# Kernel optimization log

Measured on AMD Instinct MI355X. Metric: run time of the kernel, lower is better.

## Reference

```python
import jax, jax.numpy as jnp
import numpy as np


def _init(key, shape, fan_in):
    return jax.random.normal(key, shape, jnp.float32) * (1.0 / np.sqrt(fan_in))


def setup_inputs() -> dict:
    key = jax.random.key(0)
    ks = jax.random.split(key, 12)
    b, n, vd, ad, sd, hd = 32, 2048, 512, 128, 128, 64
    return {
        'vfeat': jax.random.normal(ks[0], (b, n, vd), jnp.float32),
        'afeat': jax.random.normal(ks[1], (b, n, ad), jnp.float32),
        'vfc_w': _init(ks[2], (ad, vd), vd), 'vfc_b': jnp.zeros((ad,), jnp.float32),
        'afc_w': _init(ks[3], (ad, ad), ad), 'afc_b': jnp.zeros((ad,), jnp.float32),
        'am_v_w': _init(ks[4], (sd, sd), sd), 'am_v_b': jnp.zeros((sd,), jnp.float32),
        'am_a_w': _init(ks[5], (sd, sd), sd), 'am_a_b': jnp.zeros((sd,), jnp.float32),
        'am_o_w': _init(ks[6], (1, sd), sd), 'am_o_b': jnp.zeros((1,), jnp.float32),
        'V_w': _init(ks[7], (hd, sd), sd), 'V_b': jnp.zeros((hd,), jnp.float32),
        'W_w': _init(ks[8], (1, hd), hd), 'W_b': jnp.zeros((1,), jnp.float32),
        'cls_w': _init(ks[9], (2, sd), sd), 'cls_b': jnp.zeros((2,), jnp.float32),
    }


def reference(vfeat, afeat, vfc_w, vfc_b, afc_w, afc_b,
              am_v_w, am_v_b, am_a_w, am_a_b, am_o_w, am_o_b,
              V_w, V_b, W_w, W_b, cls_w, cls_b):
    relu = jax.nn.relu
    # vfc / afc projections (dropout is identity in eval mode)
    vo1 = relu(jnp.einsum('bnd,kd->bnk', vfeat, vfc_w) + vfc_b)  # (b,n,128)
    ax = relu(jnp.einsum('bnd,kd->bnk', afeat, afc_w) + afc_b)   # (b,n,128)
    # AM(128): additive gated cross-modal attention: out = sigmoid(Wo tanh(Wv v + Wa a)) * a
    h = jnp.tanh(jnp.einsum('bnk,jk->bnj', vo1, am_v_w) + am_v_b
                 + jnp.einsum('bnk,jk->bnj', ax, am_a_w) + am_a_b)
    att = jax.nn.sigmoid(jnp.einsum('bnj,oj->bno', h, am_o_w) + am_o_b)  # (b,n,1)
    ffeat = att * ax + vo1  # attfeat + vo1, (b,n,128)
    # NOTE: original uses self.V for BOTH f_v and f_u (source bug kept)
    f_v = relu(jnp.einsum('bnk,hk->bnh', ffeat, V_w) + V_b)  # (b,n,64)
    f_u = f_v
    # W is affine with no nonlinearity on (fv_i + fu_j), so
    # W(fv_i + fu_j) = w.fv_i + w.fu_j + b  -- exact rank-1 decomposition
    s_v = f_v @ W_w[0]  # (b,n)
    s_u = f_u @ W_w[0]  # (b,n)
    pair = s_v[:, :, None] + s_u[:, None, :] + W_b[0]  # (b,n_i,n_j)
    p = jax.nn.softmax(pair, axis=1)  # F.softmax(scores, 0) per bag: over i
    scores = p.mean(axis=2)  # mean over j -> (b,n)
    # eval mode: training-only softmax over dim 2 skipped
    zfeat = jnp.einsum('bn,bnk->bk', scores, ffeat)  # (b,128)
    logits = zfeat @ cls_w.T + cls_b  # (b,2)
    return scores, logits
```

## Files before the change

kernel.cpp:

```cpp
#include <hip/hip_runtime.h>
#include <cstddef>
#include <cstdint>


typedef __attribute__((ext_vector_type(8))) short short8;
typedef __attribute__((ext_vector_type(4))) float float4v;

#define MFMA16(a, b, c) __builtin_amdgcn_mfma_f32_16x16x32_bf16((a), (b), (c), 0, 0, 0)

__device__ __forceinline__ unsigned short f2bf(float f) {
    union { float f; unsigned u; } v; v.f = f;
    unsigned r = (v.u + 0x7fffu + ((v.u >> 16) & 1u)) >> 16;
    return (unsigned short)r;
}
__device__ __forceinline__ float bf2f(unsigned short h) {
    union { unsigned u; float f; } v; v.u = ((unsigned)h) << 16;
    return v.f;
}
__device__ __forceinline__ float bf2f_s(short h) { return bf2f((unsigned short)h); }

__device__ __forceinline__ void bfsplit(float x, short& h, short& l) {
    union { float f; unsigned u; } v; v.f = x;
    h = (short)(v.u >> 16);
    union { unsigned u; float f; } hv; hv.u = v.u & 0xffff0000u;
    union { float f; unsigned u; } lv; lv.f = x - hv.f;
    l = (short)(lv.u >> 16);
}

__device__ __forceinline__ float tanh_fast(float x) {
    float e = __builtin_exp2f(x * 2.885390081777927f);
    return 1.f - 2.f / (e + 1.f);
}
__device__ __forceinline__ float sigmoid_fast(float x) {
    return 1.f / (1.f + __builtin_exp2f(-x * 1.4426950408889634f));
}

__device__ __forceinline__ void gload_lds16(const void* g, void* l) {
#if __has_builtin(__builtin_amdgcn_global_load_lds)
    __builtin_amdgcn_global_load_lds(
        (const __attribute__((address_space(1))) unsigned int*)g,
        (__attribute__((address_space(3))) unsigned int*)l, 16, 0, 0);
#else
    *(uint4*)l = *(const uint4*)g;
#endif
}

__global__ __launch_bounds__(256)
void prep(const float* __restrict__ vfc_w, const float* __restrict__ afc_w,
          const float* __restrict__ am_v_w, const float* __restrict__ am_a_w,
          const float* __restrict__ V_w,
          unsigned short* __restrict__ W1h, unsigned short* __restrict__ W1l,
          unsigned short* __restrict__ W1bh, unsigned short* __restrict__ W1bl,
          unsigned short* __restrict__ W2v, unsigned short* __restrict__ W2a,
          unsigned short* __restrict__ W3)
{
    int t = blockIdx.x * 256 + threadIdx.x;
    if (t < 65536) {
        int j = t & 7, lane = (t >> 3) & 63, ks = (t >> 9) & 15, nf = (t >> 13) & 7;
        int n = (lane & 15) + 16 * nf, k = ks * 32 + (lane >> 4) * 8 + j;
        float x = vfc_w[n * 512 + k];
        unsigned short h = f2bf(x);
        W1h[t] = h; W1l[t] = f2bf(x - bf2f(h));
    } else if (t < 81920) {
        int u = t - 65536;
        int j = u & 7, lane = (u >> 3) & 63, ks = (u >> 9) & 3, nf = (u >> 11) & 7;
        int n = (lane & 15) + 16 * nf, k = ks * 32 + (lane >> 4) * 8 + j;
        float x = afc_w[n * 128 + k];
        unsigned short h = f2bf(x);
        W1bh[u] = h; W1bl[u] = f2bf(x - bf2f(h));
    } else if (t < 98304) {
        int u = t - 81920;
        int j = u & 7, lane = (u >> 3) & 63, ks = (u >> 9) & 3, nf = (u >> 11) & 7;
        int n = (lane & 15) + 16 * nf, k = ks * 32 + (lane >> 4) * 8 + j;
        W2v[u] = f2bf(am_v_w[n * 128 + k]);
    } else if (t < 114688) {
        int u = t - 98304;
        int j = u & 7, lane = (u >> 3) & 63, ks = (u >> 9) & 3, nf = (u >> 11) & 7;
        int n = (lane & 15) + 16 * nf, k = ks * 32 + (lane >> 4) * 8 + j;
        W2a[u] = f2bf(am_a_w[n * 128 + k]);
    } else if (t < 122880) {
        int u = t - 114688;
        int j = u & 7, lane = (u >> 3) & 63, ks = (u >> 9) & 3, nf = (u >> 11) & 3;
        int n = (lane & 15) + 16 * nf, k = ks * 32 + (lane >> 4) * 8 + j;
        W3[u] = f2bf(V_w[n * 128 + k]);
    }
}

__global__ __launch_bounds__(256, 4)
void milA1(const float* __restrict__ vfeat, const float* __restrict__ vfc_b,
           const unsigned short* __restrict__ W1h,
           const unsigned short* __restrict__ W1l,
           float* __restrict__ vo1f)
{
    __shared__ __align__(16) unsigned short Abuf[2][4096];

    const int tid = threadIdx.x;
    const int lane = tid & 63, wid = tid >> 6;
    const int lr = lane & 15, lg = lane >> 4;
    const int rowbase = blockIdx.x * 64;
    const int nf0 = wid * 2;

    const float* sap = vfeat + (size_t)(rowbase + wid * 16 + (lane >> 2)) * 512
                       + (lane & 3) * 8;
    const int dlane = (lane >> 2) + 16 * (lane & 3);
    unsigned short* dh = &Abuf[0][0] + (wid * 2 + 0) * 512 + dlane * 8;
    unsigned short* dl = dh + 512;

    auto stage_write = [&](const float4 x0, const float4 x1, int buf) {
        const float xs[8] = {x0.x, x0.y, x0.z, x0.w, x1.x, x1.y, x1.z, x1.w};
        short8 h8, l8;
#pragma unroll
        for (int j = 0; j < 8; ++j) {
            short h, l; bfsplit(xs[j], h, l);
            h8[j] = h; l8[j] = l;
        }
        *(short8*)(dh + buf * 4096) = h8;
        *(short8*)(dl + buf * 4096) = l8;
    };

    float4v acc[4][2];
#pragma unroll
    for (int rf = 0; rf < 4; ++rf)
#pragma unroll
        for (int c = 0; c < 2; ++c)
#pragma unroll
            for (int i = 0; i < 4; ++i) acc[rf][c][i] = 0.f;

    {
        float4 x0 = *(const float4*)(sap);
        float4 x1 = *(const float4*)(sap + 4);
        stage_write(x0, x1, 0);
    }
    __syncthreads();

    for (int ks = 0; ks < 16; ++ks) {
        const int cur = ks & 1;
        float4 nx0, nx1;
        if (ks < 15) {
            nx0 = *(const float4*)(sap + (ks + 1) * 32);
            nx1 = *(const float4*)(sap + (ks + 1) * 32 + 4);
        }
        const short8 b0h = *(const short8*)(W1h + ((size_t)((nf0 + 0) * 16 + ks) * 64 + lane) * 8);
        const short8 b0l = *(const short8*)(W1l + ((size_t)((nf0 + 0) * 16 + ks) * 64 + lane) * 8);
        const short8 b1h = *(const short8*)(W1h + ((size_t)((nf0 + 1) * 16 + ks) * 64 + lane) * 8);
        const short8 b1l = *(const short8*)(W1l + ((size_t)((nf0 + 1) * 16 + ks) * 64 + lane) * 8);

#pragma unroll
        for (int rf = 0; rf < 4; ++rf) {
            const short8 ah = *(const short8*)&Abuf[cur][(rf * 2 + 0) * 512 + lane * 8];
            const short8 al = *(const short8*)&Abuf[cur][(rf * 2 + 1) * 512 + lane * 8];
            acc[rf][0] = MFMA16(ah, b0h, acc[rf][0]);
            acc[rf][0] = MFMA16(ah, b0l, acc[rf][0]);
            acc[rf][0] = MFMA16(al, b0h, acc[rf][0]);
            acc[rf][1] = MFMA16(ah, b1h, acc[rf][1]);
            acc[rf][1] = MFMA16(ah, b1l, acc[rf][1]);
            acc[rf][1] = MFMA16(al, b1h, acc[rf][1]);
        }
        if (ks < 15) stage_write(nx0, nx1, cur ^ 1);
        __syncthreads();
    }

#pragma unroll
    for (int c = 0; c < 2; ++c) {
        const float bb = vfc_b[lr + 16 * (nf0 + c)];
#pragma unroll
        for (int rf = 0; rf < 4; ++rf)
#pragma unroll
            for (int r = 0; r < 4; ++r)
                vo1f[(size_t)(rowbase + rf * 16 + lg * 4 + r) * 128 + lr + 16 * (nf0 + c)] =
                    fmaxf(acc[rf][c][r] + bb, 0.f);
    }
}

__global__ __launch_bounds__(256, 3)
void milA2(const float* __restrict__ afeat,
           const float* __restrict__ afc_b,
           const float* __restrict__ am_v_b, const float* __restrict__ am_a_b,
           const float* __restrict__ am_o_w, const float* __restrict__ am_o_b,
           const float* __restrict__ V_b, const float* __restrict__ W_w,
           const unsigned short* __restrict__ W1bh, const unsigned short* __restrict__ W1bl,
           const unsigned short* __restrict__ W2v, const unsigned short* __restrict__ W2a,
           const unsigned short* __restrict__ W3,
           float* vof,
           float* __restrict__ s_out)
{
    __shared__ __align__(16) unsigned short vo1s[8192];
    __shared__ __align__(16) unsigned short axs[8192];
    __shared__ __align__(16) unsigned short bstage[8192];

    const int tid = threadIdx.x;
    const int lane = tid & 63, wid = tid >> 6;
    const int lr = lane & 15, lg = lane >> 4;
    const int row0 = blockIdx.x * 64 + wid * 16;

    float vo1r[8][4];
#pragma unroll
    for (int nf = 0; nf < 8; ++nf)
#pragma unroll
        for (int r = 0; r < 4; ++r) {
            const float v = vof[(size_t)(row0 + lg * 4 + r) * 128 + lr + 16 * nf];
            vo1r[nf][r] = v;
            const int row = lg * 4 + r;
            const int col = lr + 16 * nf;
            vo1s[wid * 2048 + row * 128 + (col ^ ((row & 7) << 3))] = f2bf(v);
        }

    float4v acc1b[8];
#pragma unroll
    for (int nf = 0; nf < 8; ++nf)
#pragma unroll
        for (int i = 0; i < 4; ++i) acc1b[nf][i] = 0.f;

    {
        const float* ap = afeat + (size_t)(row0 + lr) * 128 + lg * 8;
        float4 a0[2], a1[2], a2[2];
        a0[0] = *(const float4*)(ap);      a0[1] = *(const float4*)(ap + 4);
        a1[0] = *(const float4*)(ap + 32); a1[1] = *(const float4*)(ap + 36);

        for (int ks = 0; ks < 4; ++ks) {
            __syncthreads();
#pragma unroll
            for (int i = 0; i < 4; ++i) {
                const int f = wid * 4 + i;
                const int nf = f & 7;
                const unsigned short* src = ((f >> 3) ? W1bl : W1bh)
                    + (size_t)(nf * 4 + ks) * 512 + (size_t)lane * 8;
                gload_lds16(src, &bstage[f * 512 + lane * 8]);
            }
            __syncthreads();

            if (ks < 2) {
                a2[0] = *(const float4*)(ap + (ks + 2) * 32);
                a2[1] = *(const float4*)(ap + (ks + 2) * 32 + 4);
            }
            short8 ah, al;
            {
                const float xs[8] = {a0[0].x, a0[0].y, a0[0].z, a0[0].w,
                                     a0[1].x, a0[1].y, a0[1].z, a0[1].w};
#pragma unroll
                for (int j = 0; j < 8; ++j) {
                    short h, l; bfsplit(xs[j], h, l);
                    ah[j] = h; al[j] = l;
                }
            }
#pragma unroll
            for (int nf = 0; nf < 8; ++nf) {
                const short8 bh = *(const short8*)&bstage[nf * 512 + lane * 8];
                const short8 bl = *(const short8*)&bstage[(8 + nf) * 512 + lane * 8];
                acc1b[nf] = MFMA16(ah, bh, acc1b[nf]);
                acc1b[nf] = MFMA16(ah, bl, acc1b[nf]);
                acc1b[nf] = MFMA16(al, bh, acc1b[nf]);
            }
            a0[0] = a1[0]; a0[1] = a1[1];
            a1[0] = a2[0]; a1[1] = a2[1];
        }
    }
#pragma unroll
    for (int nf = 0; nf < 8; ++nf) {
        const float bb = afc_b[lr + 16 * nf];
#pragma unroll
        for (int r = 0; r < 4; ++r) {
            float v = fmaxf(acc1b[nf][r] + bb, 0.f);
            acc1b[nf][r] = v;
            const int row = lg * 4 + r;
            const int col = lr + 16 * nf;
            axs[wid * 2048 + row * 128 + (col ^ ((row & 7) << 3))] = f2bf(v);
        }
    }

    float4v acc2[8];
#pragma unroll
    for (int nf = 0; nf < 8; ++nf)
#pragma unroll
        for (int i = 0; i < 4; ++i) acc2[nf][i] = 0.f;

    for (int ks = 0; ks < 4; ++ks) {
        __syncthreads();
#pragma unroll
        for (int i = 0; i < 4; ++i) {
            const int f = wid * 4 + i;
            const int nf = f & 7;
            const unsigned short* src = ((f >> 3) ? W2a : W2v)
                + (size_t)(nf * 4 + ks) * 512 + (size_t)lane * 8;
            gload_lds16(src, &bstage[f * 512 + lane * 8]);
        }
        __syncthreads();
        const int rdoff = (ks * 32 + lg * 8) ^ ((lr & 7) << 3);
        const short8 a2v = *(const short8*)&vo1s[wid * 2048 + lr * 128 + rdoff];
        const short8 a2a = *(const short8*)&axs[wid * 2048 + lr * 128 + rdoff];
#pragma unroll
        for (int nf = 0; nf < 8; ++nf) {
            const short8 bv = *(const short8*)&bstage[nf * 512 + lane * 8];
            const short8 ba = *(const short8*)&bstage[(8 + nf) * 512 + lane * 8];
            acc2[nf] = MFMA16(a2v, bv, acc2[nf]);
            acc2[nf] = MFMA16(a2a, ba, acc2[nf]);
        }
    }

    __syncthreads();
#pragma unroll
    for (int i = 0; i < 4; ++i) {
        const int f = wid * 4 + i;
        gload_lds16(W3 + (size_t)f * 512 + lane * 8, &bstage[f * 512 + lane * 8]);
    }

    float attc[4];
    {
        float bias2[8], wo[8];
#pragma unroll
        for (int nf = 0; nf < 8; ++nf) {
            const int c = lr + 16 * nf;
            bias2[nf] = am_v_b[c] + am_a_b[c];
            wo[nf] = am_o_w[c];
        }
        const float ob = am_o_b[0];
#pragma unroll
        for (int r = 0; r < 4; ++r) {
            float p = 0.f;
#pragma unroll
            for (int nf = 0; nf < 8; ++nf)
                p += tanh_fast(acc2[nf][r] + bias2[nf]) * wo[nf];
            p += __shfl_xor(p, 1);
            p += __shfl_xor(p, 2);
            p += __shfl_xor(p, 4);
            p += __shfl_xor(p, 8);
            attc[r] = sigmoid_fast(p + ob);
        }
    }

#pragma unroll
    for (int nf = 0; nf < 8; ++nf)
#pragma unroll
        for (int r = 0; r < 4; ++r)
            vof[(size_t)(row0 + lg * 4 + r) * 128 + lr + 16 * nf] =
                attc[r] * acc1b[nf][r] + vo1r[nf][r];

    float attv;
    {
        const int srcl = (lr >> 2) << 4;
        const float b0 = __shfl(attc[0], srcl);
        const float b1 = __shfl(attc[1], srcl);
        const float b2 = __shfl(attc[2], srcl);
        const float b3 = __shfl(attc[3], srcl);
        attv = (lr & 2) ? ((lr & 1) ? b3 : b2) : ((lr & 1) ? b1 : b0);
    }

    __syncthreads();

    float4v acc3[4];
#pragma unroll
    for (int nf = 0; nf < 4; ++nf)
#pragma unroll
        for (int i = 0; i < 4; ++i) acc3[nf][i] = 0.f;

#pragma unroll
    for (int ks = 0; ks < 4; ++ks) {
        const int rdoff = (ks * 32 + lg * 8) ^ ((lr & 7) << 3);
        const short8 x8 = *(const short8*)&axs[wid * 2048 + lr * 128 + rdoff];
        const short8 v8 = *(const short8*)&vo1s[wid * 2048 + lr * 128 + rdoff];
        short8 a3;
#pragma unroll
        for (int j = 0; j < 8; ++j) {
            float f = attv * bf2f_s(x8[j]) + bf2f_s(v8[j]);
            a3[j] = (short)f2bf(f);
        }
#pragma unroll
        for (int nf = 0; nf < 4; ++nf) {
            const short8 b = *(const short8*)&bstage[(nf * 4 + ks) * 512 + lane * 8];
            acc3[nf] = MFMA16(a3, b, acc3[nf]);
        }
    }

    {
        float vb3[4], ww3[4];
#pragma unroll
        for (int nf = 0; nf < 4; ++nf) {
            const int c = lr + 16 * nf;
            vb3[nf] = V_b[c];
            ww3[nf] = W_w[c];
        }
#pragma unroll
        for (int r = 0; r < 4; ++r) {
            float q = 0.f;
#pragma unroll
            for (int nf = 0; nf < 4; ++nf)
                q += fmaxf(acc3[nf][r] + vb3[nf], 0.f) * ww3[nf];
            q += __shfl_xor(q, 1);
            q += __shfl_xor(q, 2);
            q += __shfl_xor(q, 4);
            q += __shfl_xor(q, 8);
            if (lr == 0) s_out[row0 + lg * 4 + r] = q;
        }
    }
}

__device__ __forceinline__ float wred_sum(float v) {
#pragma unroll
    for (int m = 32; m >= 1; m >>= 1) v += __shfl_xor(v, m);
    return v;
}
__device__ __forceinline__ float wred_max(float v) {
#pragma unroll
    for (int m = 32; m >= 1; m >>= 1) v = fmaxf(v, __shfl_xor(v, m));
    return v;
}

__global__ __launch_bounds__(256)
void milB1(const float* __restrict__ s_in, float* __restrict__ scores_out)
{
    __shared__ float red[4];
    const int t = threadIdx.x, b = blockIdx.x, w = t >> 6;
    const float* sb = s_in + (size_t)b * 2048;

    float v[8];
#pragma unroll
    for (int q = 0; q < 8; ++q) v[q] = sb[q * 256 + t];
    float m = v[0];
#pragma unroll
    for (int q = 1; q < 8; ++q) m = fmaxf(m, v[q]);
    m = wred_max(m);
    if ((t & 63) == 0) red[w] = m;
    __syncthreads();
    const float bm = fmaxf(fmaxf(red[0], red[1]), fmaxf(red[2], red[3]));

    float e[8], sum = 0.f;
#pragma unroll
    for (int q = 0; q < 8; ++q) { e[q] = expf(v[q] - bm); sum += e[q]; }
    sum = wred_sum(sum);
    __syncthreads();
    if ((t & 63) == 0) red[w] = sum;
    __syncthreads();
    const float inv = 1.f / (red[0] + red[1] + red[2] + red[3]);
#pragma unroll
    for (int q = 0; q < 8; ++q)
        scores_out[(size_t)b * 2048 + q * 256 + t] = e[q] * inv;
}

__global__ __launch_bounds__(256)
void milB2(const float* __restrict__ scores, const float* __restrict__ ffeat,
           float* __restrict__ parts)
{
    __shared__ float sh[256];
    __shared__ float zbuf[256];
    const int t = threadIdx.x;
    const int b = blockIdx.x >> 3, part = blockIdx.x & 7;
    const int col = t & 127, half = t >> 7;

    sh[t] = scores[(size_t)b * 2048 + part * 256 + t];
    __syncthreads();

    const float* fb = ffeat + ((size_t)(b * 2048 + part * 256 + half * 128)) * 128 + col;
    const float* sp = sh + half * 128;
    float z = 0.f;
#pragma unroll 8
    for (int nn = 0; nn < 128; ++nn) z += sp[nn] * fb[(size_t)nn * 128];
    zbuf[t] = z;
    __syncthreads();
    if (t < 128) parts[((size_t)(b * 8 + part)) * 128 + t] = zbuf[t] + zbuf[t + 128];
}

__global__ __launch_bounds__(128)
void milB3(const float* __restrict__ parts, const float* __restrict__ cls_w,
           const float* __restrict__ cls_b, float* __restrict__ logits)
{
    __shared__ float zfs[128];
    const int t = threadIdx.x, b = blockIdx.x;
    float zf = 0.f;
#pragma unroll
    for (int p = 0; p < 8; ++p) zf += parts[((size_t)(b * 8 + p)) * 128 + t];
    zfs[t] = zf;
    __syncthreads();
    const int o = t >> 6, c = t & 63;
    float q = zfs[c] * cls_w[o * 128 + c] + zfs[c + 64] * cls_w[o * 128 + c + 64];
    q = wred_sum(q);
    if (c == 0) logits[b * 2 + o] = q + cls_b[o];
}

extern "C" void kernel_launch(void* const* d_in, const int* in_sizes, int n_in,
                              void* d_out, int out_size, void* d_ws, size_t ws_size,
                              hipStream_t stream)
{
    (void)in_sizes; (void)n_in; (void)out_size; (void)ws_size;
    const float* vfeat  = (const float*)d_in[0];
    const float* afeat  = (const float*)d_in[1];
    const float* vfc_w  = (const float*)d_in[2];
    const float* vfc_b  = (const float*)d_in[3];
    const float* afc_w  = (const float*)d_in[4];
    const float* afc_b  = (const float*)d_in[5];
    const float* am_v_w = (const float*)d_in[6];
    const float* am_v_b = (const float*)d_in[7];
    const float* am_a_w = (const float*)d_in[8];
    const float* am_a_b = (const float*)d_in[9];
    const float* am_o_w = (const float*)d_in[10];
    const float* am_o_b = (const float*)d_in[11];
    const float* V_w    = (const float*)d_in[12];
    const float* V_b    = (const float*)d_in[13];
    const float* W_w    = (const float*)d_in[14];
    const float* cls_w  = (const float*)d_in[16];
    const float* cls_b  = (const float*)d_in[17];

    float* scores = (float*)d_out;
    float* logits = (float*)d_out + 32 * 2048;

    char* ws = (char*)d_ws;
    float* vof      = (float*)ws;
    float* s_ws     = (float*)(ws + 33554432);
    float* parts_ws = (float*)(ws + 33816576);
    unsigned short* W1h  = (unsigned short*)(ws + 33947648);
    unsigned short* W1l  = W1h + 65536;
    unsigned short* W1bh = W1l + 65536;
    unsigned short* W1bl = W1bh + 16384;
    unsigned short* W2v  = W1bl + 16384;
    unsigned short* W2a  = W2v + 16384;
    unsigned short* W3   = W2a + 16384;

    prep<<<480, 256, 0, stream>>>(vfc_w, afc_w, am_v_w, am_a_w, V_w,
                                  W1h, W1l, W1bh, W1bl, W2v, W2a, W3);
    milA1<<<1024, 256, 0, stream>>>(vfeat, vfc_b, W1h, W1l, vof);
    milA2<<<1024, 256, 0, stream>>>(afeat, afc_b, am_v_b, am_a_b,
                                    am_o_w, am_o_b, V_b, W_w,
                                    W1bh, W1bl, W2v, W2a, W3,
                                    vof, s_ws);
    milB1<<<32, 256, 0, stream>>>(s_ws, scores);
    milB2<<<256, 256, 0, stream>>>(scores, vof, parts_ws);
    milB3<<<32, 128, 0, stream>>>(parts_ws, cls_w, cls_b, logits);
}
```

Baseline: 95.59 us.

## Stage vfeat in two large swizzled LDS halves instead of per-k double buffer

The vfc projection kernel no longer streams 32-column slices of vfeat through a small double buffer with a barrier every k-step. Each wave now loads 16 full-row float4 chunks covering half of K, converts them to bf16 hi/lo, and writes them into a 64 KB XOR-swizzled LDS buffer. The second half is loaded while the first half is computed. This cuts the barrier count to a few per block and makes the global loads wider and more coalesced. In exchange it uses much more LDS and many more registers, so launch bounds drop from 4 to 2 blocks per CU, lowering occupancy.

Result: slower. 105.2 us (+10.1%).

```diff
diff --git a/kernel.cpp b/kernel.cpp
--- a/kernel.cpp
+++ b/kernel.cpp
@@ -4,6 +4,7 @@
 
 
 typedef __attribute__((ext_vector_type(8))) short short8;
+typedef __attribute__((ext_vector_type(4))) short shortv4;
 typedef __attribute__((ext_vector_type(4))) float float4v;
 
 #define MFMA16(a, b, c) __builtin_amdgcn_mfma_f32_16x16x32_bf16((a), (b), (c), 0, 0, 0)
@@ -86,13 +87,14 @@
     }
 }
 
-__global__ __launch_bounds__(256, 4)
+__global__ __launch_bounds__(256, 2)
 void milA1(const float* __restrict__ vfeat, const float* __restrict__ vfc_b,
            const unsigned short* __restrict__ W1h,
            const unsigned short* __restrict__ W1l,
            float* __restrict__ vo1f)
 {
-    __shared__ __align__(16) unsigned short Abuf[2][4096];
+    __shared__ __align__(16) unsigned short Ah[16384];
+    __shared__ __align__(16) unsigned short Al[16384];
 
     const int tid = threadIdx.x;
     const int lane = tid & 63, wid = tid >> 6;
@@ -100,65 +102,74 @@
     const int rowbase = blockIdx.x * 64;
     const int nf0 = wid * 2;
 
-    const float* sap = vfeat + (size_t)(rowbase + wid * 16 + (lane >> 2)) * 512
-                       + (lane & 3) * 8;
-    const int dlane = (lane >> 2) + 16 * (lane & 3);
-    unsigned short* dh = &Abuf[0][0] + (wid * 2 + 0) * 512 + dlane * 8;
-    unsigned short* dl = dh + 512;
-
-    auto stage_write = [&](const float4 x0, const float4 x1, int buf) {
-        const float xs[8] = {x0.x, x0.y, x0.z, x0.w, x1.x, x1.y, x1.z, x1.w};
-        short8 h8, l8;
-#pragma unroll
-        for (int j = 0; j < 8; ++j) {
-            short h, l; bfsplit(xs[j], h, l);
-            h8[j] = h; l8[j] = l;
-        }
-        *(short8*)(dh + buf * 4096) = h8;
-        *(short8*)(dl + buf * 4096) = l8;
+    float4v acc[4][2];
+#pragma unroll
+    for (int rf = 0; rf < 4; ++rf)
+#pragma unroll
+        for (int c = 0; c < 2; ++c)
+#pragma unroll
+            for (int i = 0; i < 4; ++i) acc[rf][c][i] = 0.f;
+
+    const float* srow = vfeat + (size_t)(rowbase + wid * 16) * 512 + lane * 4;
+
+    auto conv_write = [&](const float4* st) {
+#pragma unroll
+        for (int i = 0; i < 16; ++i) {
+            const int row = wid * 16 + i;
+            shortv4 h4, l4;
+            const float xs[4] = {st[i].x, st[i].y, st[i].z, st[i].w};
+#pragma unroll
+            for (int j = 0; j < 4; ++j) {
+                short h, l; bfsplit(xs[j], h, l);
+                h4[j] = h; l4[j] = l;
+            }
+            const int idx = row * 256 + ((lane * 4) ^ ((row & 7) << 3));
+            *(shortv4*)&Ah[idx] = h4;
+            *(shortv4*)&Al[idx] = l4;
+        }
     };
 
-    float4v acc[4][2];
-#pragma unroll
-    for (int rf = 0; rf < 4; ++rf)
-#pragma unroll
-        for (int c = 0; c < 2; ++c)
-#pragma unroll
-            for (int i = 0; i < 4; ++i) acc[rf][c][i] = 0.f;
-
-    {
-        float4 x0 = *(const float4*)(sap);
-        float4 x1 = *(const float4*)(sap + 4);
-        stage_write(x0, x1, 0);
-    }
-    __syncthreads();
-
-    for (int ks = 0; ks < 16; ++ks) {
-        const int cur = ks & 1;
-        float4 nx0, nx1;
-        if (ks < 15) {
-            nx0 = *(const float4*)(sap + (ks + 1) * 32);
-            nx1 = *(const float4*)(sap + (ks + 1) * 32 + 4);
-        }
-        const short8 b0h = *(const short8*)(W1h + ((size_t)((nf0 + 0) * 16 + ks) * 64 + lane) * 8);
-        const short8 b0l = *(const short8*)(W1l + ((size_t)((nf0 + 0) * 16 + ks) * 64 + lane) * 8);
-        const short8 b1h = *(const short8*)(W1h + ((size_t)((nf0 + 1) * 16 + ks) * 64 + lane) * 8);
-        const short8 b1l = *(const short8*)(W1l + ((size_t)((nf0 + 1) * 16 + ks) * 64 + lane) * 8);
-
-#pragma unroll
-        for (int rf = 0; rf < 4; ++rf) {
-            const short8 ah = *(const short8*)&Abuf[cur][(rf * 2 + 0) * 512 + lane * 8];
-            const short8 al = *(const short8*)&Abuf[cur][(rf * 2 + 1) * 512 + lane * 8];
-            acc[rf][0] = MFMA16(ah, b0h, acc[rf][0]);
-            acc[rf][0] = MFMA16(ah, b0l, acc[rf][0]);
-            acc[rf][0] = MFMA16(al, b0h, acc[rf][0]);
-            acc[rf][1] = MFMA16(ah, b1h, acc[rf][1]);
-            acc[rf][1] = MFMA16(ah, b1l, acc[rf][1]);
-            acc[rf][1] = MFMA16(al, b1h, acc[rf][1]);
-        }
-        if (ks < 15) stage_write(nx0, nx1, cur ^ 1);
-        __syncthreads();
-    }
+    auto compute = [&](int ss) {
+#pragma unroll
+        for (int kl = 0; kl < 8; ++kl) {
+            const int ks = ss * 8 + kl;
+            const short8 b0h = *(const short8*)(W1h + ((size_t)((nf0 + 0) * 16 + ks) * 64 + lane) * 8);
+            const short8 b0l = *(const short8*)(W1l + ((size_t)((nf0 + 0) * 16 + ks) * 64 + lane) * 8);
+            const short8 b1h = *(const short8*)(W1h + ((size_t)((nf0 + 1) * 16 + ks) * 64 + lane) * 8);
+            const short8 b1l = *(const short8*)(W1l + ((size_t)((nf0 + 1) * 16 + ks) * 64 + lane) * 8);
+#pragma unroll
+            for (int rf = 0; rf < 4; ++rf) {
+                const int row = rf * 16 + lr;
+                const int idx = row * 256 + ((kl * 32 + lg * 8) ^ ((row & 7) << 3));
+                const short8 ah = *(const short8*)&Ah[idx];
+                const short8 al = *(const short8*)&Al[idx];
+                acc[rf][0] = MFMA16(ah, b0h, acc[rf][0]);
+                acc[rf][0] = MFMA16(ah, b0l, acc[rf][0]);
+                acc[rf][0] = MFMA16(al, b0h, acc[rf][0]);
+                acc[rf][1] = MFMA16(ah, b1h, acc[rf][1]);
+                acc[rf][1] = MFMA16(ah, b1l, acc[rf][1]);
+                acc[rf][1] = MFMA16(al, b1h, acc[rf][1]);
+            }
+        }
+    };
+
+    float4 st0[16];
+#pragma unroll
+    for (int i = 0; i < 16; ++i)
+        st0[i] = *(const float4*)(srow + (size_t)i * 512);
+    conv_write(st0);
+    __syncthreads();
+
+    float4 st1[16];
+#pragma unroll
+    for (int i = 0; i < 16; ++i)
+        st1[i] = *(const float4*)(srow + (size_t)i * 512 + 256);
+
+    compute(0);
+    __syncthreads();
+    conv_write(st1);
+    __syncthreads();
+    compute(1);
 
 #pragma unroll
     for (int c = 0; c < 2; ++c) {
```
